# Optimization experiments

Measured on AMD Instinct MI355X. Metric: run time of the kernel, lower is better.

Reference implementation:

```python
import jax, jax.numpy as jnp
import numpy as np

N_NODES = 50000
N_EDGES = 800000
N_GRAPHS = 32
IN_DIM = 3
HID = 128
EDGE_DIM = 3
OUT_DIM = 40
N_LAYERS = 3
EPS = 1e-5
SLOPE = 0.2  # GATv2 leaky_relu negative_slope


def setup_inputs() -> dict:
    key = jax.random.key(0)
    ks = jax.random.split(key, 24)
    s = lambda fan: 1.0 / np.sqrt(fan)
    inp = {
        "x": jax.random.normal(ks[0], (N_NODES, IN_DIM), jnp.float32),
        "edge_attr": jax.random.normal(ks[1], (N_EDGES, EDGE_DIM), jnp.float32),
        "edge_index": jax.random.randint(ks[2], (2, N_EDGES), 0, N_NODES),
        "batch": jnp.sort(jax.random.randint(ks[3], (N_NODES,), 0, N_GRAPHS)),
        # layer 0 (in_dim -> hid, separate lin_l / lin_r)
        "W0l": jax.random.normal(ks[4], (IN_DIM, HID), jnp.float32) * s(IN_DIM),
        "W0r": jax.random.normal(ks[5], (IN_DIM, HID), jnp.float32) * s(IN_DIM),
        "We0": jax.random.normal(ks[6], (EDGE_DIM, HID), jnp.float32) * s(EDGE_DIM),
        "a0": jax.random.normal(ks[7], (HID,), jnp.float32) * s(HID),
        "b0": jnp.zeros((HID,), jnp.float32),
        "bn0_g": jnp.ones((HID,), jnp.float32),
        "bn0_b": jnp.zeros((HID,), jnp.float32),
        # layers 1..n-1 (hid -> hid, share_weights=True -> single W per layer)
        "W": jax.random.normal(ks[8], (N_LAYERS - 1, HID, HID), jnp.float32) * s(HID),
        "We": jax.random.normal(ks[9], (N_LAYERS - 1, EDGE_DIM, HID), jnp.float32) * s(EDGE_DIM),
        "a": jax.random.normal(ks[10], (N_LAYERS - 1, HID), jnp.float32) * s(HID),
        "b": jnp.zeros((N_LAYERS - 1, HID), jnp.float32),
        "bn_g": jnp.ones((N_LAYERS - 1, HID), jnp.float32),
        "bn_b": jnp.zeros((N_LAYERS - 1, HID), jnp.float32),
        # FC classifier head (Linear-ReLU-Linear)
        "fc1_W": jax.random.normal(ks[11], (HID, HID), jnp.float32) * s(HID),
        "fc1_b": jnp.zeros((HID,), jnp.float32),
        "fc2_W": jax.random.normal(ks[12], (HID, OUT_DIM), jnp.float32) * s(HID),
        "fc2_b": jnp.zeros((OUT_DIM,), jnp.float32),
    }
    return inp


def _self_loop_attr(edge_attr, dst):
    # PyG add_self_loops(fill_value='mean'): per-node mean of incoming edge_attr
    cnt = jax.ops.segment_sum(jnp.ones((edge_attr.shape[0],), edge_attr.dtype), dst, num_segments=N_NODES)
    tot = jax.ops.segment_sum(edge_attr, dst, num_segments=N_NODES)
    return tot / jnp.maximum(cnt, 1.0)[:, None]


def _gatv2(x, src, dst, eattr, Wl, Wr, We, att, bias):
    xl = x @ Wl                                   # [N,H] source transform
    xr = x @ Wr                                   # [N,H] target transform
    e = eattr @ We                                # [E2,H]
    m = jax.nn.leaky_relu(xl[src] + xr[dst] + e, SLOPE)
    logit = m @ att                               # [E2]
    lmax = jax.ops.segment_max(logit, dst, num_segments=N_NODES)
    ex = jnp.exp(logit - lmax[dst])
    den = jax.ops.segment_sum(ex, dst, num_segments=N_NODES)
    alpha = ex / den[dst]
    out = jax.ops.segment_sum(alpha[:, None] * xl[src], dst, num_segments=N_NODES)
    return out + bias


def _bn(h, g, b):
    mu = h.mean(0)
    var = jnp.mean((h - mu) ** 2, 0)
    return g * (h - mu) * jax.lax.rsqrt(var + EPS) + b


def reference(x, edge_attr, edge_index, batch, W0l, W0r, We0, a0, b0, bn0_g, bn0_b,
              W, We, a, b, bn_g, bn_b, fc1_W, fc1_b, fc2_W, fc2_b):
    src, dst = edge_index[0], edge_index[1]
    loop = jnp.arange(N_NODES)
    loop_attr = _self_loop_attr(edge_attr, dst)
    src2 = jnp.concatenate([src, loop])
    dst2 = jnp.concatenate([dst, loop])
    eattr2 = jnp.concatenate([edge_attr, loop_attr], axis=0)

    h = _gatv2(x, src2, dst2, eattr2, W0l, W0r, We0, a0, b0)
    h = _bn(jax.nn.relu(h), bn0_g, bn0_b)
    for i in range(N_LAYERS - 1):  # share_weights=True: Wl == Wr == W[i]
        h = _gatv2(h, src2, dst2, eattr2, W[i], W[i], We[i], a[i], b[i])
        h = _bn(jax.nn.relu(h), bn_g[i], bn_b[i])

    pooled = jax.ops.segment_max(h, batch, num_segments=N_GRAPHS)  # [G,H]
    z = jax.nn.relu(pooled @ fc1_W + fc1_b)
    return z @ fc2_W + fc2_b  # [G, OUT_DIM]
```

## Files before the change

### kernel.cpp

```cpp
#include <hip/hip_runtime.h>

#define NN 50000
#define NE 800000
#define NG 32
#define HID 128
#define BNEPS 1e-5f
#define NETOT (NE + NN)

typedef float f32x2 __attribute__((ext_vector_type(2)));

__device__ __forceinline__ unsigned fenc(float f) {
  unsigned u = __float_as_uint(f);
  return (u & 0x80000000u) ? ~u : (u | 0x80000000u);
}

__device__ __forceinline__ unsigned bfr(float f) {
  unsigned u = __float_as_uint(f);
  return (u + 0x7fffu + ((u >> 16) & 1u)) >> 16;
}
__device__ __forceinline__ unsigned pack2(float a, float b) {
  return bfr(a) | (bfr(b) << 16);
}
__device__ __forceinline__ float bf_lo(unsigned u) { return __uint_as_float(u << 16); }
__device__ __forceinline__ float bf_hi(unsigned u) { return __uint_as_float(u & 0xffff0000u); }

#define DPPADD(x, ctrl, rmask)                                                   \
  (x) += __int_as_float(__builtin_amdgcn_update_dpp(0, __float_as_int(x),        \
                                                    (ctrl), (rmask), 0xf, true))


__global__ __launch_bounds__(256) void k_hist(const int* __restrict__ ei,
                                              int* __restrict__ deg,
                                              int* __restrict__ pos) {
  int e = blockIdx.x * 256 + threadIdx.x;
  if (e >= NE) return;
  pos[e] = atomicAdd(&deg[ei[NE + e]], 1);
}

__global__ __launch_bounds__(1024) void k_scanA(const int* __restrict__ deg,
                                                int* __restrict__ rowp,
                                                int* __restrict__ bsum) {
  __shared__ int wsum[16];
  int t = threadIdx.x, lane = t & 63, w = t >> 6;
  int i = blockIdx.x * 1024 + t;
  int v = (i < NN) ? (deg[i] + 1) : 0;
  int s = v;
#pragma unroll
  for (int off = 1; off < 64; off <<= 1) {
    int y = __shfl_up(s, off, 64);
    if (lane >= off) s += y;
  }
  if (lane == 63) wsum[w] = s;
  __syncthreads();
  if (t < 16) {
    int xv = wsum[t];
#pragma unroll
    for (int off = 1; off < 16; off <<= 1) {
      int y = __shfl_up(xv, off, 64);
      if (t >= off) xv += y;
    }
    wsum[t] = xv;
  }
  __syncthreads();
  int wexcl = (w == 0) ? 0 : wsum[w - 1];
  int incl = wexcl + s;
  if (i < NN) rowp[i] = incl - v;
  if (t == 1023) bsum[blockIdx.x] = incl;
}

__global__ __launch_bounds__(64) void k_scanB(int* __restrict__ bsum,
                                              int* __restrict__ rowp,
                                              uint2* __restrict__ edat) {
  int t = threadIdx.x;
  int v = (t < 49) ? bsum[t] : 0;
  int s = v;
#pragma unroll
  for (int off = 1; off < 64; off <<= 1) {
    int y = __shfl_up(s, off, 64);
    if (t >= off) s += y;
  }
  bsum[t] = s - v;
  if (t == 48) rowp[NN] = s;
  for (int j = t; j < 256; j += 64) {
    uint2 z; z.x = 0u; z.y = 0u;
    edat[NETOT + j] = z;
  }
}

__global__ __launch_bounds__(1024) void k_scanC(int* __restrict__ rowp,
                                                const int* __restrict__ bsum) {
  int i = blockIdx.x * 1024 + threadIdx.x;
  if (i < NN) rowp[i] += bsum[blockIdx.x];
}

__global__ __launch_bounds__(256) void k_scatter(const int* __restrict__ ei,
    const float* __restrict__ eattr, const int* __restrict__ rowp,
    const int* __restrict__ pos, uint2* __restrict__ edat) {
  int e = blockIdx.x * 256 + threadIdx.x;
  if (e >= NE) return;
  int d = ei[NE + e];
  int p = rowp[d] + pos[e];
  uint2 v;
  v.x = (unsigned)ei[e] | (bfr(eattr[e * 3 + 0]) << 16);
  v.y = bfr(eattr[e * 3 + 1]) | (bfr(eattr[e * 3 + 2]) << 16);
  edat[p] = v;
}

__global__ __launch_bounds__(256) void k_selfmean(const int* __restrict__ rowp,
                                                  uint2* __restrict__ edat) {
  int n = blockIdx.x * 256 + threadIdx.x;
  if (n >= NN) return;
  int beg = rowp[n], endm1 = rowp[n + 1] - 1;
  float s0 = 0.f, s1 = 0.f, s2 = 0.f;
  for (int i = beg; i < endm1; ++i) {
    uint2 v = edat[i];
    s0 += bf_hi(v.x); s1 += bf_lo(v.y); s2 += bf_hi(v.y);
  }
  int cnt = endm1 - beg;
  float inv = cnt > 0 ? 1.f / (float)cnt : 0.f;
  uint2 o;
  o.x = (unsigned)n | (bfr(s0 * inv) << 16);
  o.y = bfr(s1 * inv) | (bfr(s2 * inv) << 16);
  edat[endm1] = o;
}


__global__ __launch_bounds__(256) void k_xform0(const float* __restrict__ x,
    const float* __restrict__ W0l, const float* __restrict__ W0r,
    unsigned* __restrict__ A, unsigned* __restrict__ B) {
  int t = blockIdx.x * 256 + threadIdx.x;
  int n = t >> 5;
  int c = (t & 31) * 4;
  if (n >= NN) return;
  float x0 = x[n * 3 + 0], x1 = x[n * 3 + 1], x2 = x[n * 3 + 2];
  float4 a0 = *(const float4*)&W0l[c];
  float4 a1 = *(const float4*)&W0l[HID + c];
  float4 a2 = *(const float4*)&W0l[2 * HID + c];
  float oax = x0 * a0.x + x1 * a1.x + x2 * a2.x;
  float oay = x0 * a0.y + x1 * a1.y + x2 * a2.y;
  float oaz = x0 * a0.z + x1 * a1.z + x2 * a2.z;
  float oaw = x0 * a0.w + x1 * a1.w + x2 * a2.w;
  uint2 pa;
  pa.x = pack2(oax, oay);
  pa.y = pack2(oaz, oaw);
  *(uint2*)&A[n * 64 + (c >> 1)] = pa;
  float4 b0 = *(const float4*)&W0r[c];
  float4 b1 = *(const float4*)&W0r[HID + c];
  float4 b2 = *(const float4*)&W0r[2 * HID + c];
  float obx = x0 * b0.x + x1 * b1.x + x2 * b2.x;
  float oby = x0 * b0.y + x1 * b1.y + x2 * b2.y;
  float obz = x0 * b0.z + x1 * b1.z + x2 * b2.z;
  float obw = x0 * b0.w + x1 * b1.w + x2 * b2.w;
  uint2 pb;
  pb.x = pack2(obx, oby);
  pb.y = pack2(obz, obw);
  *(uint2*)&B[n * 64 + (c >> 1)] = pb;
}


__global__ __launch_bounds__(256) void k_gemm(const unsigned* __restrict__ Hb,
    const float* __restrict__ W, const float* __restrict__ cs,
    const float* __restrict__ g, const float* __restrict__ b,
    unsigned* __restrict__ A) {
  extern __shared__ float lds[];
  float* hs = lds;
  float* Ws = lds + 32 * HID;
  int t = threadIdx.x;
  for (int i = t * 4; i < HID * HID; i += 1024)
    *(float4*)&Ws[i] = *(const float4*)&W[i];
  int rl = t >> 5;
  int c4 = (t & 31) * 4;
  float4 s1v = *(const float4*)&cs[c4];
  float4 s2v = *(const float4*)&cs[HID + c4];
  float4 gv  = *(const float4*)&g[c4];
  float4 bv  = *(const float4*)&b[c4];
  float4 sc, sh;
  {
    float mu, var;
    mu = s1v.x * (1.f / NN); var = fmaxf(s2v.x * (1.f / NN) - mu * mu, 0.f);
    sc.x = gv.x * rsqrtf(var + BNEPS); sh.x = bv.x - mu * sc.x;
    mu = s1v.y * (1.f / NN); var = fmaxf(s2v.y * (1.f / NN) - mu * mu, 0.f);
    sc.y = gv.y * rsqrtf(var + BNEPS); sh.y = bv.y - mu * sc.y;
    mu = s1v.z * (1.f / NN); var = fmaxf(s2v.z * (1.f / NN) - mu * mu, 0.f);
    sc.z = gv.z * rsqrtf(var + BNEPS); sh.z = bv.z - mu * sc.z;
    mu = s1v.w * (1.f / NN); var = fmaxf(s2v.w * (1.f / NN) - mu * mu, 0.f);
    sc.w = gv.w * rsqrtf(var + BNEPS); sh.w = bv.w - mu * sc.w;
  }
  for (int r0 = blockIdx.x * 32; r0 < NN; r0 += gridDim.x * 32) {
    __syncthreads();
#pragma unroll
    for (int j = 0; j < 4; ++j) {
      int row = rl + 8 * j;
      int r = r0 + row;
      uint2 hv = make_uint2(0u, 0u);
      if (r < NN) hv = *(const uint2*)&Hb[r * 64 + (c4 >> 1)];
      float4 o;
      o.x = fmaxf(bf_lo(hv.x), 0.f) * sc.x + sh.x;
      o.y = fmaxf(bf_hi(hv.x), 0.f) * sc.y + sh.y;
      o.z = fmaxf(bf_lo(hv.y), 0.f) * sc.z + sh.z;
      o.w = fmaxf(bf_hi(hv.y), 0.f) * sc.w + sh.w;
      *(float4*)&hs[row * HID + c4] = o;
    }
    __syncthreads();
    float4 a0 = make_float4(0.f, 0.f, 0.f, 0.f);
    float4 a1 = a0, a2 = a0, a3 = a0;
#pragma unroll 4
    for (int k4 = 0; k4 < HID; k4 += 4) {
      float4 w0 = *(float4*)&Ws[(k4 + 0) * HID + c4];
      float4 w1 = *(float4*)&Ws[(k4 + 1) * HID + c4];
      float4 w2 = *(float4*)&Ws[(k4 + 2) * HID + c4];
      float4 w3 = *(float4*)&Ws[(k4 + 3) * HID + c4];
      float4 h;
      h = *(float4*)&hs[(rl + 0) * HID + k4];
      a0.x += h.x*w0.x + h.y*w1.x + h.z*w2.x + h.w*w3.x;
      a0.y += h.x*w0.y + h.y*w1.y + h.z*w2.y + h.w*w3.y;
      a0.z += h.x*w0.z + h.y*w1.z + h.z*w2.z + h.w*w3.z;
      a0.w += h.x*w0.w + h.y*w1.w + h.z*w2.w + h.w*w3.w;
      h = *(float4*)&hs[(rl + 8) * HID + k4];
      a1.x += h.x*w0.x + h.y*w1.x + h.z*w2.x + h.w*w3.x;
      a1.y += h.x*w0.y + h.y*w1.y + h.z*w2.y + h.w*w3.y;
      a1.z += h.x*w0.z + h.y*w1.z + h.z*w2.z + h.w*w3.z;
      a1.w += h.x*w0.w + h.y*w1.w + h.z*w2.w + h.w*w3.w;
      h = *(float4*)&hs[(rl + 16) * HID + k4];
      a2.x += h.x*w0.x + h.y*w1.x + h.z*w2.x + h.w*w3.x;
      a2.y += h.x*w0.y + h.y*w1.y + h.z*w2.y + h.w*w3.y;
      a2.z += h.x*w0.z + h.y*w1.z + h.z*w2.z + h.w*w3.z;
      a2.w += h.x*w0.w + h.y*w1.w + h.z*w2.w + h.w*w3.w;
      h = *(float4*)&hs[(rl + 24) * HID + k4];
      a3.x += h.x*w0.x + h.y*w1.x + h.z*w2.x + h.w*w3.x;
      a3.y += h.x*w0.y + h.y*w1.y + h.z*w2.y + h.w*w3.y;
      a3.z += h.x*w0.z + h.y*w1.z + h.z*w2.z + h.w*w3.z;
      a3.w += h.x*w0.w + h.y*w1.w + h.z*w2.w + h.w*w3.w;
    }
    int r = r0 + rl;
    int ci = c4 >> 1;
    if (r < NN) {
      uint2 p; p.x = pack2(a0.x, a0.y); p.y = pack2(a0.z, a0.w);
      *(uint2*)&A[r * 64 + ci] = p;
    }
    if (r + 8 < NN) {
      uint2 p; p.x = pack2(a1.x, a1.y); p.y = pack2(a1.z, a1.w);
      *(uint2*)&A[(r + 8) * 64 + ci] = p;
    }
    if (r + 16 < NN) {
      uint2 p; p.x = pack2(a2.x, a2.y); p.y = pack2(a2.z, a2.w);
      *(uint2*)&A[(r + 16) * 64 + ci] = p;
    }
    if (r + 24 < NN) {
      uint2 p; p.x = pack2(a3.x, a3.y); p.y = pack2(a3.z, a3.w);
      *(uint2*)&A[(r + 24) * 64 + ci] = p;
    }
  }
}


__global__ __launch_bounds__(256) void k_edge(const unsigned* __restrict__ XL,
    const unsigned* __restrict__ XR, const uint2* __restrict__ edat,
    const int* __restrict__ rowp, const float* __restrict__ We,
    const float* __restrict__ att, const float* __restrict__ bias,
    unsigned* __restrict__ Hb) {
  __shared__ float WeS[3 * HID];
  int t = threadIdx.x;
  for (int i = t; i < 3 * HID; i += 256) WeS[i] = We[i];
  __syncthreads();
  int lane = t & 63;
  int l5 = lane & 31;
  int half = lane >> 5;
  int n = blockIdx.x * 8 + (t >> 6) * 2 + half;
  int c0 = l5 * 4;
  uint2 urx = *(const uint2*)&XR[n * 64 + l5 * 2];
  f32x2 xr01 = {bf_lo(urx.x), bf_hi(urx.x)};
  f32x2 xr23 = {bf_lo(urx.y), bf_hi(urx.y)};
  f32x2 at01 = *(const f32x2*)&att[c0];
  f32x2 at23 = *(const f32x2*)&att[c0 + 2];
  at01 *= 1.44269504f;
  at23 *= 1.44269504f;
  f32x2 w0a = {WeS[c0], WeS[c0 + 1]},               w0b = {WeS[c0 + 2], WeS[c0 + 3]};
  f32x2 w1a = {WeS[HID + c0], WeS[HID + c0 + 1]},   w1b = {WeS[HID + c0 + 2], WeS[HID + c0 + 3]};
  f32x2 w2a = {WeS[2*HID + c0], WeS[2*HID + c0+1]}, w2b = {WeS[2*HID + c0+2], WeS[2*HID + c0+3]};
  int beg = rowp[n], end = rowp[n + 1];
  int rem = end - beg;
  int tc = max(rem, __shfl_xor(rem, 32, 64));
  int trips = (__builtin_amdgcn_readfirstlane(tc) + 3) & ~3;
  const unsigned* XLg = XL + l5 * 2;

  uint2 e0 = edat[beg], e1 = edat[beg + 1], e2 = edat[beg + 2], e3 = edat[beg + 3];
  uint2 x0 = *(const uint2*)&XLg[(e0.x & 0xffffu) * 64];
  uint2 x1 = *(const uint2*)&XLg[(e1.x & 0xffffu) * 64];
  uint2 x2, x3;
  f32x2 a01 = {0.f, 0.f}, a23 = {0.f, 0.f};
  float s = 0.f;

#define BODY(ED, XU, J)                                                           \
  {                                                                               \
    f32x2 xs01 = {bf_lo(XU.x), bf_hi(XU.x)};                                      \
    f32x2 xs23 = {bf_lo(XU.y), bf_hi(XU.y)};                                      \
    float ea0 = bf_hi(ED.x), ea1 = bf_lo(ED.y), ea2 = bf_hi(ED.y);                \
    f32x2 u01 = xs01 + xr01;                                                      \
    f32x2 u23 = xs23 + xr23;                                                      \
    u01 = ea0 * w0a + u01;  u23 = ea0 * w0b + u23;                                \
    u01 = ea1 * w1a + u01;  u23 = ea1 * w1b + u23;                                \
    u01 = ea2 * w2a + u01;  u23 = ea2 * w2b + u23;                                \
    f32x2 v01 = __builtin_elementwise_max(u01, 0.2f * u01);                       \
    f32x2 v23 = __builtin_elementwise_max(u23, 0.2f * u23);                       \
    f32x2 pl = v01 * at01 + v23 * at23;                                           \
    float part = pl.x + pl.y;                                                     \
    DPPADD(part, 0x111, 0xf);                                                     \
    DPPADD(part, 0x112, 0xf);                                                     \
    DPPADD(part, 0x114, 0xf);                                                     \
    DPPADD(part, 0x118, 0xf);                                                     \
    DPPADD(part, 0x142, 0xa);                                                     \
    part = __int_as_float(__builtin_amdgcn_ds_swizzle(                            \
        __float_as_int(part), 0x3E0));          \
    float p = __builtin_amdgcn_exp2f(part);                                       \
    p = (i + (J) < rem) ? p : 0.f;                                                \
    s += p;                                                                       \
    a01 = p * xs01 + a01;                                                         \
    a23 = p * xs23 + a23;                                                         \
  }

  for (int i = 0; i < trips; i += 4) {
    x2 = *(const uint2*)&XLg[(e2.x & 0xffffu) * 64];
    BODY(e0, x0, 0);
    e0 = edat[beg + i + 4];
    x3 = *(const uint2*)&XLg[(e3.x & 0xffffu) * 64];
    BODY(e1, x1, 1);
    e1 = edat[beg + i + 5];
    x0 = *(const uint2*)&XLg[(e0.x & 0xffffu) * 64];
    BODY(e2, x2, 2);
    e2 = edat[beg + i + 6];
    x1 = *(const uint2*)&XLg[(e1.x & 0xffffu) * 64];
    BODY(e3, x3, 3);
    e3 = edat[beg + i + 7];
  }
#undef BODY

  float inv = 1.f / s;
  f32x2 b01 = *(const f32x2*)&bias[c0];
  f32x2 b23 = *(const f32x2*)&bias[c0 + 2];
  f32x2 o01 = a01 * inv + b01;
  f32x2 o23 = a23 * inv + b23;
  uint2 o;
  o.x = pack2(o01.x, o01.y);
  o.y = pack2(o23.x, o23.y);
  *(uint2*)&Hb[n * 64 + l5 * 2] = o;
}


__global__ __launch_bounds__(256) void k_bnstats(const unsigned* __restrict__ Hb,
                                                 float* __restrict__ cs) {
  __shared__ float red[8][256];
  int t = threadIdx.x;
  int ui = (t & 31) * 2;
  int c0 = ui * 2;
  int grp = t >> 5;
  int chunk = (NN + gridDim.x - 1) / gridDim.x;
  int n0 = blockIdx.x * chunk, n1 = min(n0 + chunk, NN);
  float s10 = 0.f, s11 = 0.f, s12 = 0.f, s13 = 0.f;
  float s20 = 0.f, s21 = 0.f, s22 = 0.f, s23 = 0.f;
  for (int n = n0 + grp; n < n1; n += 8) {
    uint2 h = *(const uint2*)&Hb[n * 64 + ui];
    float v0 = fmaxf(bf_lo(h.x), 0.f), v1 = fmaxf(bf_hi(h.x), 0.f);
    float v2 = fmaxf(bf_lo(h.y), 0.f), v3 = fmaxf(bf_hi(h.y), 0.f);
    s10 += v0; s11 += v1; s12 += v2; s13 += v3;
    s20 += v0 * v0; s21 += v1 * v1; s22 += v2 * v2; s23 += v3 * v3;
  }
  red[grp][c0 + 0] = s10; red[grp][c0 + 1] = s11;
  red[grp][c0 + 2] = s12; red[grp][c0 + 3] = s13;
  red[grp][128 + c0 + 0] = s20; red[grp][128 + c0 + 1] = s21;
  red[grp][128 + c0 + 2] = s22; red[grp][128 + c0 + 3] = s23;
  __syncthreads();
  float sum = 0.f;
#pragma unroll
  for (int g2 = 0; g2 < 8; ++g2) sum += red[g2][t];
  atomicAdd(&cs[t], sum);
}


__global__ __launch_bounds__(256) void k_pool(const unsigned* __restrict__ Hb,
    const int* __restrict__ batch, const float* __restrict__ cs,
    const float* __restrict__ g, const float* __restrict__ b,
    unsigned* __restrict__ pooled) {
  int t = threadIdx.x;
  int ui = (t & 31) * 2;
  int c0 = ui * 2;
  int grp = t >> 5;
  float scv0, scv1, scv2, scv3, shv0, shv1, shv2, shv3;
  {
    float mu, var;
    mu = cs[c0 + 0] * (1.f / NN); var = fmaxf(cs[HID + c0 + 0] * (1.f / NN) - mu * mu, 0.f);
    scv0 = g[c0 + 0] * rsqrtf(var + BNEPS); shv0 = b[c0 + 0] - mu * scv0;
    mu = cs[c0 + 1] * (1.f / NN); var = fmaxf(cs[HID + c0 + 1] * (1.f / NN) - mu * mu, 0.f);
    scv1 = g[c0 + 1] * rsqrtf(var + BNEPS); shv1 = b[c0 + 1] - mu * scv1;
    mu = cs[c0 + 2] * (1.f / NN); var = fmaxf(cs[HID + c0 + 2] * (1.f / NN) - mu * mu, 0.f);
    scv2 = g[c0 + 2] * rsqrtf(var + BNEPS); shv2 = b[c0 + 2] - mu * scv2;
    mu = cs[c0 + 3] * (1.f / NN); var = fmaxf(cs[HID + c0 + 3] * (1.f / NN) - mu * mu, 0.f);
    scv3 = g[c0 + 3] * rsqrtf(var + BNEPS); shv3 = b[c0 + 3] - mu * scv3;
  }
  int chunk = (NN + gridDim.x - 1) / gridDim.x;
  int n0 = blockIdx.x * chunk, n1 = min(n0 + chunk, NN);
  int curg = -1;
  float m0 = -3.402823e38f, m1 = m0, m2 = m0, m3 = m0;
  for (int n = n0 + grp; n < n1; n += 8) {
    int gg = batch[n];
    if (gg != curg) {
      if (curg >= 0) {
        atomicMax(&pooled[curg * HID + c0 + 0], fenc(m0));
        atomicMax(&pooled[curg * HID + c0 + 1], fenc(m1));
        atomicMax(&pooled[curg * HID + c0 + 2], fenc(m2));
        atomicMax(&pooled[curg * HID + c0 + 3], fenc(m3));
      }
      curg = gg;
      m0 = m1 = m2 = m3 = -3.402823e38f;
    }
    uint2 h = *(const uint2*)&Hb[n * 64 + ui];
    m0 = fmaxf(m0, fmaxf(bf_lo(h.x), 0.f) * scv0 + shv0);
    m1 = fmaxf(m1, fmaxf(bf_hi(h.x), 0.f) * scv1 + shv1);
    m2 = fmaxf(m2, fmaxf(bf_lo(h.y), 0.f) * scv2 + shv2);
    m3 = fmaxf(m3, fmaxf(bf_hi(h.y), 0.f) * scv3 + shv3);
  }
  if (curg >= 0) {
    atomicMax(&pooled[curg * HID + c0 + 0], fenc(m0));
    atomicMax(&pooled[curg * HID + c0 + 1], fenc(m1));
    atomicMax(&pooled[curg * HID + c0 + 2], fenc(m2));
    atomicMax(&pooled[curg * HID + c0 + 3], fenc(m3));
  }
}


__global__ __launch_bounds__(128) void k_fc(const unsigned* __restrict__ pooled,
    const float* __restrict__ W1, const float* __restrict__ b1,
    const float* __restrict__ W2, const float* __restrict__ b2,
    float* __restrict__ out) {
  __shared__ float P[HID];
  __shared__ float Z[HID];
  int g = blockIdx.x, c = threadIdx.x;
  unsigned k = pooled[g * HID + c];
  P[c] = (k & 0x80000000u) ? __uint_as_float(k ^ 0x80000000u) : __uint_as_float(~k);
  __syncthreads();
  float acc = b1[c];
  for (int kk = 0; kk < HID; ++kk) acc += P[kk] * W1[kk * HID + c];
  Z[c] = fmaxf(acc, 0.f);
  __syncthreads();
  if (c < 40) {
    float a2 = b2[c];
    for (int kk = 0; kk < HID; ++kk) a2 += Z[kk] * W2[kk * 40 + c];
    out[g * 40 + c] = a2;
  }
}


extern "C" void kernel_launch(void* const* d_in, const int* in_sizes, int n_in,
                              void* d_out, int out_size, void* d_ws, size_t ws_size,
                              hipStream_t stream) {
  (void)in_sizes; (void)n_in; (void)out_size; (void)ws_size;
  const float* x     = (const float*)d_in[0];
  const float* eattr = (const float*)d_in[1];
  const int*   ei    = (const int*)d_in[2];
  const int*   batch = (const int*)d_in[3];
  const float* W0l   = (const float*)d_in[4];
  const float* W0r   = (const float*)d_in[5];
  const float* We0   = (const float*)d_in[6];
  const float* a0    = (const float*)d_in[7];
  const float* b0    = (const float*)d_in[8];
  const float* bn0g  = (const float*)d_in[9];
  const float* bn0b  = (const float*)d_in[10];
  const float* Wl    = (const float*)d_in[11];
  const float* Wel   = (const float*)d_in[12];
  const float* al    = (const float*)d_in[13];
  const float* bl    = (const float*)d_in[14];
  const float* bng   = (const float*)d_in[15];
  const float* bnb   = (const float*)d_in[16];
  const float* fc1W  = (const float*)d_in[17];
  const float* fc1b  = (const float*)d_in[18];
  const float* fc2W  = (const float*)d_in[19];
  const float* fc2b  = (const float*)d_in[20];
  float* out = (float*)d_out;

  char* ws = (char*)d_ws;
  unsigned* Hbf  = (unsigned*)(ws + 0);
  unsigned* Abf  = (unsigned*)(ws + 12800000);
  unsigned* X0bf = (unsigned*)(ws + 25600000);
  uint2*    edat = (uint2*)(ws + 38400000);
  int*      rowp = (int*)(ws + 45202048);
  int*      pos  = (int*)(ws + 45402112);
  char*     zb   = ws + 48602112;
  int*      deg  = (int*)(zb + 0);
  float*    cs   = (float*)(zb + 200000);
  unsigned* pooled = (unsigned*)(zb + 203072);
  int*      bsum = (int*)(zb + 219456);
  const size_t ZLEN = 219712;

  hipMemsetAsync(zb, 0, ZLEN, stream);

  k_hist<<<(NE + 255) / 256, 256, 0, stream>>>(ei, deg, pos);
  k_scanA<<<49, 1024, 0, stream>>>(deg, rowp, bsum);
  k_scanB<<<1, 64, 0, stream>>>(bsum, rowp, edat);
  k_scanC<<<49, 1024, 0, stream>>>(rowp, bsum);
  k_scatter<<<(NE + 255) / 256, 256, 0, stream>>>(ei, eattr, rowp, pos, edat);
  k_selfmean<<<(NN + 255) / 256, 256, 0, stream>>>(rowp, edat);

  const size_t GEMM_LDS = (size_t)(32 * HID + HID * HID) * 4;

  k_xform0<<<(NN * 32) / 256, 256, 0, stream>>>(x, W0l, W0r, Abf, X0bf);
  k_edge<<<NN / 8, 256, 0, stream>>>(Abf, X0bf, edat, rowp, We0, a0, b0, Hbf);
  k_bnstats<<<512, 256, 0, stream>>>(Hbf, cs);

  k_gemm<<<782, 256, GEMM_LDS, stream>>>(Hbf, Wl, cs, bn0g, bn0b, Abf);
  k_edge<<<NN / 8, 256, 0, stream>>>(Abf, Abf, edat, rowp, Wel, al, bl, Hbf);
  k_bnstats<<<512, 256, 0, stream>>>(Hbf, cs + 256);

  k_gemm<<<782, 256, GEMM_LDS, stream>>>(Hbf, Wl + 128 * 128, cs + 256, bng, bnb, Abf);
  k_edge<<<NN / 8, 256, 0, stream>>>(Abf, Abf, edat, rowp, Wel + 384, al + 128, bl + 128, Hbf);
  k_bnstats<<<512, 256, 0, stream>>>(Hbf, cs + 512);

  k_pool<<<512, 256, 0, stream>>>(Hbf, batch, cs + 512, bng + 128, bnb + 128, pooled);
  k_fc<<<NG, 128, 0, stream>>>(pooled, fc1W, fc1b, fc2W, fc2b, out);
}
```

Baseline: 398.0 us.

## Run hidden-layer GEMM on bf16 MFMA with batch-norm folded into weights

Replaces the scalar FP32 LDS-tiled 128x128 node GEMM with MFMA 16x16x32 bf16 instructions. A new single-block prep kernel folds the batch-norm scale into a transposed bf16 copy of the weights and turns the shift into a per-column bias. ReLU is applied by masking negative bf16 halves in place. This cuts FP32 FMA work and LDS traffic in the GEMM, at the cost of an extra small launch per layer and bf16 rounding of the scaled weights.

```diff
diff --git a/kernel.cpp b/kernel.cpp
--- a/kernel.cpp
+++ b/kernel.cpp
@@ -8,6 +8,8 @@
 #define NETOT (NE + NN)
 
 typedef float f32x2 __attribute__((ext_vector_type(2)));
+typedef float f32x4 __attribute__((ext_vector_type(4)));
+typedef short bf16x8 __attribute__((ext_vector_type(8)));
 
 __device__ __forceinline__ unsigned fenc(float f) {
   unsigned u = __float_as_uint(f);
@@ -158,97 +160,74 @@
 }
 
 
+__global__ __launch_bounds__(256) void k_wprep(const float* __restrict__ W,
+    const float* __restrict__ cs, const float* __restrict__ g,
+    const float* __restrict__ b, unsigned* __restrict__ Wt,
+    float* __restrict__ bias2) {
+  __shared__ float scS[HID], shS[HID];
+  int t = threadIdx.x;
+  if (t < HID) {
+    float mu = cs[t] * (1.f / NN);
+    float var = fmaxf(cs[HID + t] * (1.f / NN) - mu * mu, 0.f);
+    float sc = g[t] * rsqrtf(var + BNEPS);
+    scS[t] = sc;
+    shS[t] = b[t] - mu * sc;
+  }
+  __syncthreads();
+  for (int i = t; i < HID * 64; i += 256) {
+    int n = i >> 6, kp = (i & 63) * 2;
+    Wt[i] = pack2(scS[kp] * W[kp * HID + n], scS[kp + 1] * W[(kp + 1) * HID + n]);
+  }
+  if (t < HID) {
+    float acc = 0.f;
+    for (int k = 0; k < HID; ++k) acc += shS[k] * W[k * HID + t];
+    bias2[t] = acc;
+  }
+}
+
+
 __global__ __launch_bounds__(256) void k_gemm(const unsigned* __restrict__ Hb,
-    const float* __restrict__ W, const float* __restrict__ cs,
-    const float* __restrict__ g, const float* __restrict__ b,
+    const unsigned* __restrict__ Wt, const float* __restrict__ bias2,
     unsigned* __restrict__ A) {
-  extern __shared__ float lds[];
-  float* hs = lds;
-  float* Ws = lds + 32 * HID;
+  __shared__ unsigned WsL[HID * 68];
   int t = threadIdx.x;
-  for (int i = t * 4; i < HID * HID; i += 1024)
-    *(float4*)&Ws[i] = *(const float4*)&W[i];
-  int rl = t >> 5;
-  int c4 = (t & 31) * 4;
-  float4 s1v = *(const float4*)&cs[c4];
-  float4 s2v = *(const float4*)&cs[HID + c4];
-  float4 gv  = *(const float4*)&g[c4];
-  float4 bv  = *(const float4*)&b[c4];
-  float4 sc, sh;
-  {
-    float mu, var;
-    mu = s1v.x * (1.f / NN); var = fmaxf(s2v.x * (1.f / NN) - mu * mu, 0.f);
-    sc.x = gv.x * rsqrtf(var + BNEPS); sh.x = bv.x - mu * sc.x;
-    mu = s1v.y * (1.f / NN); var = fmaxf(s2v.y * (1.f / NN) - mu * mu, 0.f);
-    sc.y = gv.y * rsqrtf(var + BNEPS); sh.y = bv.y - mu * sc.y;
-    mu = s1v.z * (1.f / NN); var = fmaxf(s2v.z * (1.f / NN) - mu * mu, 0.f);
-    sc.z = gv.z * rsqrtf(var + BNEPS); sh.z = bv.z - mu * sc.z;
-    mu = s1v.w * (1.f / NN); var = fmaxf(s2v.w * (1.f / NN) - mu * mu, 0.f);
-    sc.w = gv.w * rsqrtf(var + BNEPS); sh.w = bv.w - mu * sc.w;
-  }
-  for (int r0 = blockIdx.x * 32; r0 < NN; r0 += gridDim.x * 32) {
-    __syncthreads();
-#pragma unroll
-    for (int j = 0; j < 4; ++j) {
-      int row = rl + 8 * j;
-      int r = r0 + row;
-      uint2 hv = make_uint2(0u, 0u);
-      if (r < NN) hv = *(const uint2*)&Hb[r * 64 + (c4 >> 1)];
-      float4 o;
-      o.x = fmaxf(bf_lo(hv.x), 0.f) * sc.x + sh.x;
-      o.y = fmaxf(bf_hi(hv.x), 0.f) * sc.y + sh.y;
-      o.z = fmaxf(bf_lo(hv.y), 0.f) * sc.z + sh.z;
-      o.w = fmaxf(bf_hi(hv.y), 0.f) * sc.w + sh.w;
-      *(float4*)&hs[row * HID + c4] = o;
+  for (int i = t; i < HID * 64; i += 256)
+    WsL[(i >> 6) * 68 + (i & 63)] = Wt[i];
+  __syncthreads();
+  int l = t & 63;
+  int w = t >> 6;
+  int r0 = blockIdx.x * 64 + w * 16;
+  int l15 = l & 15;
+  int arow = min(r0 + l15, NN - 1);
+  int kg = (l >> 4) * 4;
+  float bl[8];
+#pragma unroll
+  for (int nt = 0; nt < 8; ++nt) bl[nt] = bias2[nt * 16 + l15];
+  f32x4 acc[8] = {};
+#pragma unroll
+  for (int ks = 0; ks < 4; ++ks) {
+    uint4 au = *(const uint4*)&Hb[arow * 64 + ks * 16 + kg];
+    au.x &= ~(((au.x >> 15) & 0x10001u) * 0xFFFFu);
+    au.y &= ~(((au.y >> 15) & 0x10001u) * 0xFFFFu);
+    au.z &= ~(((au.z >> 15) & 0x10001u) * 0xFFFFu);
+    au.w &= ~(((au.w >> 15) & 0x10001u) * 0xFFFFu);
+    bf16x8 af = *(bf16x8*)&au;
+#pragma unroll
+    for (int nt = 0; nt < 8; ++nt) {
+      uint4 bu = *(const uint4*)&WsL[(nt * 16 + l15) * 68 + ks * 16 + kg];
+      bf16x8 bf = *(bf16x8*)&bu;
+      acc[nt] = __builtin_amdgcn_mfma_f32_16x16x32_bf16(af, bf, acc[nt], 0, 0, 0);
     }
-    __syncthreads();
-    float4 a0 = make_float4(0.f, 0.f, 0.f, 0.f);
-    float4 a1 = a0, a2 = a0, a3 = a0;
-#pragma unroll 4
-    for (int k4 = 0; k4 < HID; k4 += 4) {
-      float4 w0 = *(float4*)&Ws[(k4 + 0) * HID + c4];
-      float4 w1 = *(float4*)&Ws[(k4 + 1) * HID + c4];
-      float4 w2 = *(float4*)&Ws[(k4 + 2) * HID + c4];
-      float4 w3 = *(float4*)&Ws[(k4 + 3) * HID + c4];
-      float4 h;
-      h = *(float4*)&hs[(rl + 0) * HID + k4];
-      a0.x += h.x*w0.x + h.y*w1.x + h.z*w2.x + h.w*w3.x;
-      a0.y += h.x*w0.y + h.y*w1.y + h.z*w2.y + h.w*w3.y;
-      a0.z += h.x*w0.z + h.y*w1.z + h.z*w2.z + h.w*w3.z;
-      a0.w += h.x*w0.w + h.y*w1.w + h.z*w2.w + h.w*w3.w;
-      h = *(float4*)&hs[(rl + 8) * HID + k4];
-      a1.x += h.x*w0.x + h.y*w1.x + h.z*w2.x + h.w*w3.x;
-      a1.y += h.x*w0.y + h.y*w1.y + h.z*w2.y + h.w*w3.y;
-      a1.z += h.x*w0.z + h.y*w1.z + h.z*w2.z + h.w*w3.z;
-      a1.w += h.x*w0.w + h.y*w1.w + h.z*w2.w + h.w*w3.w;
-      h = *(float4*)&hs[(rl + 16) * HID + k4];
-      a2.x += h.x*w0.x + h.y*w1.x + h.z*w2.x + h.w*w3.x;
-      a2.y += h.x*w0.y + h.y*w1.y + h.z*w2.y + h.w*w3.y;
-      a2.z += h.x*w0.z + h.y*w1.z + h.z*w2.z + h.w*w3.z;
-      a2.w += h.x*w0.w + h.y*w1.w + h.z*w2.w + h.w*w3.w;
-      h = *(float4*)&hs[(rl + 24) * HID + k4];
-      a3.x += h.x*w0.x + h.y*w1.x + h.z*w2.x + h.w*w3.x;
-      a3.y += h.x*w0.y + h.y*w1.y + h.z*w2.y + h.w*w3.y;
-      a3.z += h.x*w0.z + h.y*w1.z + h.z*w2.z + h.w*w3.z;
-      a3.w += h.x*w0.w + h.y*w1.w + h.z*w2.w + h.w*w3.w;
-    }
-    int r = r0 + rl;
-    int ci = c4 >> 1;
-    if (r < NN) {
-      uint2 p; p.x = pack2(a0.x, a0.y); p.y = pack2(a0.z, a0.w);
-      *(uint2*)&A[r * 64 + ci] = p;
-    }
-    if (r + 8 < NN) {
-      uint2 p; p.x = pack2(a1.x, a1.y); p.y = pack2(a1.z, a1.w);
-      *(uint2*)&A[(r + 8) * 64 + ci] = p;
-    }
-    if (r + 16 < NN) {
-      uint2 p; p.x = pack2(a2.x, a2.y); p.y = pack2(a2.z, a2.w);
-      *(uint2*)&A[(r + 16) * 64 + ci] = p;
-    }
-    if (r + 24 < NN) {
-      uint2 p; p.x = pack2(a3.x, a3.y); p.y = pack2(a3.z, a3.w);
-      *(uint2*)&A[(r + 24) * 64 + ci] = p;
+  }
+#pragma unroll
+  for (int nt = 0; nt < 8; ++nt) {
+#pragma unroll
+    for (int reg = 0; reg < 4; ++reg) {
+      float v = acc[nt][reg] + bl[nt];
+      float nb = __shfl_down(v, 1, 64);
+      int rm = r0 + (l >> 4) * 4 + reg;
+      if (((l & 1) == 0) && rm < NN)
+        A[rm * 64 + nt * 8 + (l15 >> 1)] = pack2(v, nb);
     }
   }
 }
@@ -490,6 +469,8 @@
   unsigned* pooled = (unsigned*)(zb + 203072);
   int*      bsum = (int*)(zb + 219456);
   const size_t ZLEN = 219712;
+  unsigned* wtb   = (unsigned*)(ws + 48821824);
+  float*    bias2 = (float*)(ws + 48854592);
 
   hipMemsetAsync(zb, 0, ZLEN, stream);
 
@@ -500,17 +481,17 @@
   k_scatter<<<(NE + 255) / 256, 256, 0, stream>>>(ei, eattr, rowp, pos, edat);
   k_selfmean<<<(NN + 255) / 256, 256, 0, stream>>>(rowp, edat);
 
-  const size_t GEMM_LDS = (size_t)(32 * HID + HID * HID) * 4;
-
   k_xform0<<<(NN * 32) / 256, 256, 0, stream>>>(x, W0l, W0r, Abf, X0bf);
   k_edge<<<NN / 8, 256, 0, stream>>>(Abf, X0bf, edat, rowp, We0, a0, b0, Hbf);
   k_bnstats<<<512, 256, 0, stream>>>(Hbf, cs);
 
-  k_gemm<<<782, 256, GEMM_LDS, stream>>>(Hbf, Wl, cs, bn0g, bn0b, Abf);
+  k_wprep<<<1, 256, 0, stream>>>(Wl, cs, bn0g, bn0b, wtb, bias2);
+  k_gemm<<<(NN + 63) / 64, 256, 0, stream>>>(Hbf, wtb, bias2, Abf);
   k_edge<<<NN / 8, 256, 0, stream>>>(Abf, Abf, edat, rowp, Wel, al, bl, Hbf);
   k_bnstats<<<512, 256, 0, stream>>>(Hbf, cs + 256);
 
-  k_gemm<<<782, 256, GEMM_LDS, stream>>>(Hbf, Wl + 128 * 128, cs + 256, bng, bnb, Abf);
+  k_wprep<<<1, 256, 0, stream>>>(Wl + 128 * 128, cs + 256, bng, bnb, wtb, bias2);
+  k_gemm<<<(NN + 63) / 64, 256, 0, stream>>>(Hbf, wtb, bias2, Abf);
   k_edge<<<NN / 8, 256, 0, stream>>>(Abf, Abf, edat, rowp, Wel + 384, al + 128, bl + 128, Hbf);
   k_bnstats<<<512, 256, 0, stream>>>(Hbf, cs + 512);
 
```

After: 352.2 us. -11.5%, faster.
